# Performance work log

Hardware: AMD Instinct MI355X
Metric: run time of the kernel (lower is better)

The kernel has to match this reference:

```python
import jax, jax.numpy as jnp
import numpy as np

K = 4096          # input_size
N = 12288         # output_size
M = 4096          # tokens (batch*seq)
GROUP_SIZE = 128  # EXL2 quantization group size along K
G = K // GROUP_SIZE


def setup_inputs() -> dict:
    key = jax.random.key(0)
    k1, k2, k3, k4, k5 = jax.random.split(key, 5)
    input_ = jax.random.normal(k1, (M, K), dtype=jnp.float16)
    # packed 4-bit weights: 8 nibbles per int32 along K -> [K//8, N]
    q_weight = jax.random.randint(k2, (K // 8, N), 0, 2147483647, dtype=jnp.int32)
    # packed 4-bit scale codes: 8 per int32 along N -> [G, N//8]
    q_scale = jax.random.randint(k3, (G, N // 8), 0, 2147483647, dtype=jnp.int32)
    # per-group max scale (post_init divides by 256)
    q_scale_max = (jax.random.uniform(k4, (G,), dtype=jnp.float32) / 256.0).astype(jnp.float16)
    q_invperm = jax.random.permutation(k5, jnp.arange(K, dtype=jnp.int32))
    bias = jnp.zeros((N,), dtype=jnp.float16)
    return {"input_": input_, "q_weight": q_weight, "q_scale": q_scale,
            "q_scale_max": q_scale_max, "q_invperm": q_invperm, "bias": bias}


def _dequant(q_weight, q_scale, q_scale_max):
    # unpack 8 4-bit weight codes per int32 along K
    shifts = jnp.arange(8, dtype=jnp.int32) * 4
    wn = (q_weight[:, None, :] >> shifts[None, :, None]) & 0xF   # [K//8, 8, N]
    wn = wn.reshape(K, N).astype(jnp.float32)
    # unpack 8 4-bit scale codes per int32 along N
    sn = (q_scale[:, :, None] >> shifts[None, None, :]) & 0xF    # [G, N//8, 8]
    sn = sn.reshape(G, N).astype(jnp.float32)
    # exllamav2 scale law: s = (code + 1)^2 * scale_max (per group)
    scale = (sn + 1.0) ** 2 * q_scale_max.astype(jnp.float32)[:, None]  # [G, N]
    scale = jnp.repeat(scale, GROUP_SIZE, axis=0)                # [K, N]
    return (wn - 8.0) * scale                                    # dequantized fp32 [K, N]


def reference(input_, q_weight, q_scale, q_scale_max, q_invperm, bias):
    W = _dequant(q_weight, q_scale, q_scale_max)                 # [K, N] fp32
    perm = jnp.argsort(q_invperm)                                # q_perm from post_init
    x = input_.astype(jnp.float32)[:, perm]                      # permuted activations [M, K]
    out = jnp.matmul(x, W).astype(jnp.float16)                   # fused dequant-GEMM result
    return out + bias
```

## Files before the change

kernel.cpp:

```cpp
#include <hip/hip_runtime.h>

#define Mdim 4096
#define Kdim 4096
#define Ndim 12288

typedef __bf16 bf16x8 __attribute__((ext_vector_type(8)));
typedef float f32x4 __attribute__((ext_vector_type(4)));
typedef unsigned short u16x8 __attribute__((ext_vector_type(8)));
typedef int i32x4 __attribute__((ext_vector_type(4)));

__device__ __forceinline__ unsigned short f2bf(float f) {
    unsigned int u = __builtin_bit_cast(unsigned int, f);
    u += 0x7FFFu + ((u >> 16) & 1u);
    return (unsigned short)(u >> 16);
}

typedef __attribute__((address_space(1))) void gvoid_t;
typedef __attribute__((address_space(3))) void lvoid_t;
__device__ __forceinline__ void gld16(const void* g, void* l) {
    __builtin_amdgcn_global_load_lds((gvoid_t*)g, (lvoid_t*)l, 16, 0, 0);
}


__global__ __launch_bounds__(512) void permute_convert_a_kernel(
    const float* __restrict__ A, const int* __restrict__ invperm,
    unsigned short* __restrict__ Ab)
{
    __shared__ unsigned short rowbuf[16][4104];
    const int tid = threadIdx.x;
    const int m0 = blockIdx.x * 16;
    const int bm = m0 >> 8;
    const int q  = (m0 >> 4) & 15;
#pragma unroll
    for (int c = 0; c < 2; ++c) {
        const int i = (c * 512 + tid) * 4;
        const i32x4 ip = *(const i32x4*)&invperm[i];
        for (int r = 0; r < 16; ++r) {
            const f32x4 v = *(const f32x4*)&A[(size_t)(m0 + r) * Kdim + i];
#pragma unroll
            for (int u = 0; u < 4; ++u) rowbuf[r][ip[u]] = f2bf(v[u]);
        }
    }
    __syncthreads();
    unsigned short* dst = Ab + ((size_t)bm << 20) + q * 512;
    for (int it = 0; it < 16; ++it) {
        const int c = it * 512 + tid;
        const int ks = c >> 6, c8 = c & 63;
        const u16x8 v = *(const u16x8*)&rowbuf[c8 & 15][ks * 32 + (c8 >> 4) * 8];
        *(u16x8*)&dst[(size_t)ks * 8192 + c8 * 8] = v;
    }
}

__global__ __launch_bounds__(256) void dequant_kernel(
    const int* __restrict__ qw,
    const int* __restrict__ qs,
    const float* __restrict__ qsm,
    unsigned short* __restrict__ Wt)
{
    __shared__ unsigned short tile[64 * 72];
    const int k0 = blockIdx.x * 64;
    const int n0 = blockIdx.y * 64;
    const int g = k0 >> 7;
    const int tid = threadIdx.x;
    const int n_l = tid & 63;
    const int kb_l = tid >> 6;
    const int n = n0 + n_l;
    const int sw = qs[g * (Ndim / 8) + (n >> 3)];
    const int sc = (sw >> ((n & 7) * 4)) & 0xF;
    const float scale = (float)((sc + 1) * (sc + 1)) * qsm[g];
#pragma unroll
    for (int ii = 0; ii < 2; ++ii) {
        const int kb = kb_l + ii * 4;
        const int w = qw[(size_t)(k0 / 8 + kb) * Ndim + n];
        u16x8 o;
#pragma unroll
        for (int u = 0; u < 8; ++u)
            o[u] = f2bf((float)(((w >> (4 * u)) & 0xF) - 8) * scale);
        *(u16x8*)&tile[n_l * 72 + kb * 8] = o;
    }
    __syncthreads();
    const int bn  = n0 >> 8;
    const int q0  = (n0 >> 4) & 15;
    const int ks0 = k0 >> 5;
    unsigned short* dst = Wt + ((size_t)bn << 20) + (size_t)ks0 * 8192 + q0 * 512;
#pragma unroll
    for (int cc = 0; cc < 2; ++cc) {
        const int c  = cc * 256 + tid;
        const int ksl = c >> 8;
        const int cq  = (c >> 6) & 3;
        const int c8  = c & 63;
        const u16x8 v = *(const u16x8*)
            &tile[(cq * 16 + (c8 & 15)) * 72 + ksl * 32 + (c8 >> 4) * 8];
        *(u16x8*)&dst[(size_t)ksl * 8192 + cq * 512 + c8 * 8] = v;
    }
}

#define BAR()    asm volatile("s_barrier" ::: "memory")
#define VMCNT8() asm volatile("s_waitcnt vmcnt(8)" ::: "memory")

#define STAGE(dstW, src, slot, R) do {                                      \
    gld16((src) + (size_t)(R) * 8192, (dstW) + (slot) * 8192);              \
    gld16((src) + (size_t)(R) * 8192 + 4096,                                \
          (dstW) + (slot) * 8192 + 4096); } while (0)

#define LD_A_SET(dst, slot, mh) do {                                        \
    const unsigned short* p_ = &As[slot][wm * 4096 + (mh) * 2048 + aOff];   \
    dst[0] = *(const bf16x8*)(p_);                                          \
    dst[1] = *(const bf16x8*)(p_ + 512);                                    \
    dst[2] = *(const bf16x8*)(p_ + 1024);                                   \
    dst[3] = *(const bf16x8*)(p_ + 1536); } while (0)

#define LD_B_SET(dst, slot) do {                                            \
    const unsigned short* p_ = &Bs[slot][wn * 2048 + aOff];                 \
    dst[0] = *(const bf16x8*)(p_);                                          \
    dst[1] = *(const bf16x8*)(p_ + 512);                                    \
    dst[2] = *(const bf16x8*)(p_ + 1024);                                   \
    dst[3] = *(const bf16x8*)(p_ + 1536); } while (0)

#define MFMA_SET(aset, bset, mh) do {                                       \
    __builtin_amdgcn_s_setprio(1);                                          \
    _Pragma("unroll")                                                       \
    for (int i_ = 0; i_ < 4; ++i_)                                          \
      _Pragma("unroll")                                                     \
      for (int j_ = 0; j_ < 4; ++j_)                                        \
        acc[(mh) * 4 + i_][j_] = __builtin_amdgcn_mfma_f32_16x16x32_bf16(   \
            aset[i_], bset[j_], acc[(mh) * 4 + i_][j_], 0, 0, 0);           \
    __builtin_amdgcn_s_setprio(0); } while (0)

__global__ __launch_bounds__(512, 2) void gemm_bf16_256_kernel(
    const unsigned short* __restrict__ A,
    const unsigned short* __restrict__ Bt,
    const float* __restrict__ bias,
    float* __restrict__ C)
{
    __shared__ __attribute__((aligned(16))) unsigned short As[4][8192];
    __shared__ __attribute__((aligned(16))) unsigned short Bs[4][8192];

    const int tid = threadIdx.x;
    const int lane = tid & 63, wave = tid >> 6;
    const int wm = wave >> 2, wn = wave & 3;

    const int wgid = (blockIdx.x & 7) * 96 + (blockIdx.x >> 3);
    const int bm = wgid & 15;
    const int bn = wgid >> 4;

    const unsigned short* Ag = A + ((size_t)bm << 20) + tid * 8;
    const unsigned short* Bg = Bt + ((size_t)bn << 20) + tid * 8;
    unsigned short* AsW = &As[0][0] + wave * 512;
    unsigned short* BsW = &Bs[0][0] + wave * 512;

    const int aOff = lane * 8;

    f32x4 acc[8][4];
    const f32x4 zero = {0.f, 0.f, 0.f, 0.f};
#pragma unroll
    for (int i = 0; i < 8; ++i)
#pragma unroll
        for (int j = 0; j < 4; ++j) acc[i][j] = zero;

    STAGE(AsW, Ag, 0, 0);
    STAGE(BsW, Bg, 0, 0);
    STAGE(AsW, Ag, 1, 1);
    STAGE(BsW, Bg, 1, 1);
    STAGE(AsW, Ag, 2, 2);
    STAGE(BsW, Bg, 2, 2);
    VMCNT8();
    BAR();

    bf16x8 afX[4], afY[4], bf0[4], bf1[4];
    LD_A_SET(afX, 0, 0);
    LD_B_SET(bf0, 0);

#pragma unroll 2
    for (int t = 0; t < 64; ++t) {
        const int s0 = (2 * t) & 3, s1 = (2 * t + 1) & 3;
        const int sd1 = (2 * t + 3) & 3, sA = (2 * t + 2) & 3;
        const int R1 = (2 * t + 3 < 128) ? (2 * t + 3) : 127;
        const int R2 = (2 * t + 4 < 128) ? (2 * t + 4) : 127;
        STAGE(AsW, Ag, sd1, R1);
        BAR();
        LD_A_SET(afY, s0, 1);
        MFMA_SET(afX, bf0, 0);
        BAR();
        STAGE(BsW, Bg, sd1, R1);
        VMCNT8();
        BAR();
        LD_A_SET(afX, s1, 0);
        LD_B_SET(bf1, s1);
        MFMA_SET(afY, bf0, 1);
        BAR();
        STAGE(AsW, Ag, s0, R2);
        BAR();
        LD_A_SET(afY, s1, 1);
        MFMA_SET(afX, bf1, 0);
        BAR();
        STAGE(BsW, Bg, s0, R2);
        VMCNT8();
        BAR();
        if (t < 63) {
            LD_A_SET(afX, sA, 0);
            LD_B_SET(bf0, sA);
        }
        MFMA_SET(afY, bf1, 1);
        BAR();
    }

    const int colb = bn * 256 + wn * 64 + (lane & 15);
    const int rowb = bm * 256 + wm * 128 + (lane >> 4) * 4;
    float bj[4];
#pragma unroll
    for (int j = 0; j < 4; ++j) bj[j] = bias[colb + j * 16];
#pragma unroll
    for (int mf = 0; mf < 8; ++mf)
#pragma unroll
        for (int r = 0; r < 4; ++r) {
            const size_t row = (size_t)(rowb + mf * 16 + r);
#pragma unroll
            for (int j = 0; j < 4; ++j)
                C[row * Ndim + colb + j * 16] = acc[mf][j][r] + bj[j];
        }
}

extern "C" void kernel_launch(void* const* d_in, const int* in_sizes, int n_in,
                              void* d_out, int out_size, void* d_ws, size_t ws_size,
                              hipStream_t stream) {
    const float* input   = (const float*)d_in[0];
    const int*   qw      = (const int*)d_in[1];
    const int*   qs      = (const int*)d_in[2];
    const float* qsm     = (const float*)d_in[3];
    const int*   invperm = (const int*)d_in[4];
    const float* bias    = (const float*)d_in[5];
    float*       out     = (float*)d_out;

    unsigned short* Ab = (unsigned short*)d_ws;
    unsigned short* Wt = (unsigned short*)((char*)d_ws + ((size_t)Mdim * Kdim * 2));

    permute_convert_a_kernel<<<Mdim / 16, 512, 0, stream>>>(input, invperm, Ab);
    dequant_kernel<<<dim3(Kdim / 64, Ndim / 64), 256, 0, stream>>>(qw, qs, qsm, Wt);
    gemm_bf16_256_kernel<<<dim3((Mdim / 256) * (Ndim / 256)), 512, 0, stream>>>(
        Ab, Wt, bias, out);
}
```

Baseline: 622.3 us.

## Reschedule GEMM main loop to issue LDS fragment loads earlier

```diff
diff --git a/kernel.cpp b/kernel.cpp
--- a/kernel.cpp
+++ b/kernel.cpp
@@ -97,20 +97,21 @@
 
 #define BAR()    asm volatile("s_barrier" ::: "memory")
 #define VMCNT8() asm volatile("s_waitcnt vmcnt(8)" ::: "memory")
+#define VMCNT6() asm volatile("s_waitcnt vmcnt(6)" ::: "memory")
 
 #define STAGE(dstW, src, slot, R) do {                                      \
     gld16((src) + (size_t)(R) * 8192, (dstW) + (slot) * 8192);              \
     gld16((src) + (size_t)(R) * 8192 + 4096,                                \
           (dstW) + (slot) * 8192 + 4096); } while (0)
 
-#define LD_A_SET(dst, slot, mh) do {                                        \
+#define LD_A_TO(dst, slot, mh) do {                                         \
     const unsigned short* p_ = &As[slot][wm * 4096 + (mh) * 2048 + aOff];   \
     dst[0] = *(const bf16x8*)(p_);                                          \
     dst[1] = *(const bf16x8*)(p_ + 512);                                    \
     dst[2] = *(const bf16x8*)(p_ + 1024);                                   \
     dst[3] = *(const bf16x8*)(p_ + 1536); } while (0)
 
-#define LD_B_SET(dst, slot) do {                                            \
+#define LD_B_TO(dst, slot) do {                                             \
     const unsigned short* p_ = &Bs[slot][wn * 2048 + aOff];                 \
     dst[0] = *(const bf16x8*)(p_);                                          \
     dst[1] = *(const bf16x8*)(p_ + 512);                                    \
@@ -167,41 +168,39 @@
     VMCNT8();
     BAR();
 
-    bf16x8 afX[4], afY[4], bf0[4], bf1[4];
-    LD_A_SET(afX, 0, 0);
-    LD_B_SET(bf0, 0);
+    bf16x8 aX[4], aY[4], bU[4], bV[4];
+    LD_A_TO(aX, 0, 0);
+    LD_B_TO(bU, 0);
 
 #pragma unroll 2
     for (int t = 0; t < 64; ++t) {
         const int s0 = (2 * t) & 3, s1 = (2 * t + 1) & 3;
-        const int sd1 = (2 * t + 3) & 3, sA = (2 * t + 2) & 3;
+        const int sA = (2 * t + 2) & 3, sd1 = (2 * t + 3) & 3;
         const int R1 = (2 * t + 3 < 128) ? (2 * t + 3) : 127;
         const int R2 = (2 * t + 4 < 128) ? (2 * t + 4) : 127;
+        LD_A_TO(aY, s0, 1);
         STAGE(AsW, Ag, sd1, R1);
         BAR();
-        LD_A_SET(afY, s0, 1);
-        MFMA_SET(afX, bf0, 0);
-        BAR();
+        MFMA_SET(aX, bU, 0);
+        BAR();
+        VMCNT6();
+        LD_A_TO(aX, s1, 0);
+        LD_B_TO(bV, s1);
         STAGE(BsW, Bg, sd1, R1);
-        VMCNT8();
-        BAR();
-        LD_A_SET(afX, s1, 0);
-        LD_B_SET(bf1, s1);
-        MFMA_SET(afY, bf0, 1);
-        BAR();
+        BAR();
+        MFMA_SET(aY, bU, 1);
+        BAR();
+        LD_A_TO(aY, s1, 1);
         STAGE(AsW, Ag, s0, R2);
         BAR();
-        LD_A_SET(afY, s1, 1);
-        MFMA_SET(afX, bf1, 0);
-        BAR();
+        MFMA_SET(aX, bV, 0);
+        BAR();
+        VMCNT6();
+        LD_A_TO(aX, sA, 0);
+        LD_B_TO(bU, sA);
         STAGE(BsW, Bg, s0, R2);
-        VMCNT8();
-        BAR();
-        if (t < 63) {
-            LD_A_SET(afX, sA, 0);
-            LD_B_SET(bf0, sA);
-        }
-        MFMA_SET(afY, bf1, 1);
+        BAR();
+        MFMA_SET(aY, bV, 1);
         BAR();
     }
 
```

After: 638.7 us. 1.03x slower.
